# Kernel tuning notes

Measured on AMD Instinct MI355X. Metric: run time of the kernel, lower is better.

## Reference

```python
import jax, jax.numpy as jnp
import numpy as np

DIM, HEADS, DIM_HEAD = 1024, 16, 64
INNER = HEADS * DIM_HEAD  # 1024
FF = 4 * DIM
EPS = 1e-5


def layer_norm(x, g, b):
    mu = jnp.mean(x, axis=-1, keepdims=True)
    var = jnp.mean(jnp.square(x - mu), axis=-1, keepdims=True)
    return (x - mu) * jax.lax.rsqrt(var + EPS) * g + b


def setup_inputs() -> dict:
    key = jax.random.key(0)
    ks = jax.random.split(key, 8)
    B, N = 2, 2048
    s = 0.02
    return {
        "x": jax.random.normal(ks[0], (B, N, DIM), dtype=jnp.float32),
        "ln1_g": jnp.ones((DIM,), jnp.float32),
        "ln1_b": jnp.zeros((DIM,), jnp.float32),
        "ln2_g": jnp.ones((DIM,), jnp.float32),
        "ln2_b": jnp.zeros((DIM,), jnp.float32),
        "w_qkv": jax.random.normal(ks[1], (DIM, 3 * INNER), jnp.float32) * s,
        "w_out": jax.random.normal(ks[2], (INNER, DIM), jnp.float32) * s,
        "b_out": jnp.zeros((DIM,), jnp.float32),
        "w_ff1": jax.random.normal(ks[3], (DIM, FF), jnp.float32) * s,
        "b_ff1": jnp.zeros((FF,), jnp.float32),
        "w_ff2": jax.random.normal(ks[4], (FF, DIM), jnp.float32) * s,
        "b_ff2": jnp.zeros((DIM,), jnp.float32),
    }


def reference(x, ln1_g, ln1_b, ln2_g, ln2_b, w_qkv, w_out, b_out,
              w_ff1, b_ff1, w_ff2, b_ff2):
    B, N, _ = x.shape
    scale = DIM_HEAD ** -0.5
    h = layer_norm(x, ln1_g, ln1_b)
    qkv = h @ w_qkv  # [B, N, 3*INNER]
    q, k, v = jnp.split(qkv, 3, axis=-1)
    # b n (h d) -> b h n d
    def to_heads(t):
        return t.reshape(B, N, HEADS, DIM_HEAD).transpose(0, 2, 1, 3)
    q, k, v = to_heads(q), to_heads(k), to_heads(v)
    dots = jnp.einsum('bhnd,bhmd->bhnm', q, k) * scale
    attn = jax.nn.softmax(dots, axis=-1)  # dropout = identity (eval)
    out = jnp.einsum('bhnm,bhmd->bhnd', attn, v)
    out = out.transpose(0, 2, 1, 3).reshape(B, N, INNER)
    out = out @ w_out + b_out
    x = x + out  # residual
    h2 = layer_norm(x, ln2_g, ln2_b)
    ff = jax.nn.gelu(h2 @ w_ff1 + b_ff1, approximate=False) @ w_ff2 + b_ff2
    return x + ff
```

## Files before the change

kernel.cpp:

```cpp
#include <hip/hip_runtime.h>
#include <hip/hip_bf16.h>
#include <math.h>

#define SEQ   2048
#define BATCH 2
#define NROWS 4096
#define DIMM  1024
#define QKV3  3072
#define FFD   4096
#define NHEAD 16
#define DHEAD 64

typedef __bf16 bf16;
typedef __bf16 bf16x4 __attribute__((ext_vector_type(4)));
typedef __bf16 bf16x8 __attribute__((ext_vector_type(8)));
typedef float  f32x4  __attribute__((ext_vector_type(4)));

static __device__ __forceinline__ f32x4 mfma16(bf16x8 a, bf16x8 b, f32x4 c) {
    return __builtin_amdgcn_mfma_f32_16x16x32_bf16(a, b, c, 0, 0, 0);
}

#define GLDS16(gp, lp) __builtin_amdgcn_global_load_lds( \
    (__attribute__((address_space(1))) void*)(gp),       \
    (__attribute__((address_space(3))) void*)(lp), 16, 0, 0)

#define MEMFENCE asm volatile("" ::: "memory")

__global__ __launch_bounds__(256) void wcast_kernel(
    const float* __restrict__ wqkv, bf16* __restrict__ wqkvT,
    const float* __restrict__ wout, bf16* __restrict__ woutT,
    const float* __restrict__ wff1, bf16* __restrict__ wff1T,
    const float* __restrict__ wff2, bf16* __restrict__ wff2T)
{
    int t = blockIdx.x;
    const float* src; bf16* dst; int K, N, nx;
    if (t < 3072)      { src = wqkv; dst = wqkvT; K = DIMM; N = QKV3; nx = 96;  }
    else if (t < 4096) { src = wout; dst = woutT; K = DIMM; N = DIMM; nx = 32; t -= 3072; }
    else if (t < 8192) { src = wff1; dst = wff1T; K = DIMM; N = FFD;  nx = 128; t -= 4096; }
    else               { src = wff2; dst = wff2T; K = FFD;  N = DIMM; nx = 32; t -= 8192; }
    const int k0 = (t / nx) * 32;
    const int n0 = (t - (t / nx) * nx) * 32;

    __shared__ float tile[32][33];
    const int r = threadIdx.x >> 5;
    const int c = threadIdx.x & 31;
    #pragma unroll
    for (int i = 0; i < 4; ++i)
        tile[r + 8 * i][c] = src[(size_t)(k0 + r + 8 * i) * N + n0 + c];
    __syncthreads();
    #pragma unroll
    for (int i = 0; i < 4; ++i)
        dst[(size_t)(n0 + r + 8 * i) * K + k0 + c] = (bf16)tile[c][r + 8 * i];
}

__global__ __launch_bounds__(256) void ln_cast_kernel(
    const float* __restrict__ x, const float* __restrict__ g,
    const float* __restrict__ b, bf16* __restrict__ out)
{
    const int row = blockIdx.x;
    const int t = threadIdx.x;
    const float4 v = ((const float4*)(x + (size_t)row * DIMM))[t];
    float s  = v.x + v.y + v.z + v.w;
    float sq = v.x * v.x + v.y * v.y + v.z * v.z + v.w * v.w;
    #pragma unroll
    for (int m = 1; m < 64; m <<= 1) {
        s  += __shfl_xor(s, m, 64);
        sq += __shfl_xor(sq, m, 64);
    }
    __shared__ float ss[4], ssq[4];
    const int wave = t >> 6;
    if ((t & 63) == 0) { ss[wave] = s; ssq[wave] = sq; }
    __syncthreads();
    s  = ss[0] + ss[1] + ss[2] + ss[3];
    sq = ssq[0] + ssq[1] + ssq[2] + ssq[3];
    const float mean = s * (1.0f / DIMM);
    const float var  = sq * (1.0f / DIMM) - mean * mean;
    const float rs   = rsqrtf(var + 1e-5f);
    const float4 gv = ((const float4*)g)[t];
    const float4 bv = ((const float4*)b)[t];
    bf16* o = out + (size_t)row * DIMM + t * 4;
    o[0] = (bf16)((v.x - mean) * rs * gv.x + bv.x);
    o[1] = (bf16)((v.y - mean) * rs * gv.y + bv.y);
    o[2] = (bf16)((v.z - mean) * rs * gv.z + bv.z);
    o[3] = (bf16)((v.w - mean) * rs * gv.w + bv.w);
}

template<int EPI>
__global__ __launch_bounds__(512, 2)
void gemm256_kernel(const bf16* __restrict__ A, const bf16* __restrict__ BT,
                    const float* __restrict__ bias, bf16* __restrict__ C,
                    int M, int N, int K, int ld)
{
    __shared__ bf16 As_[2][2][8192];
    __shared__ bf16 Bs_[2][2][8192];
    const int nb = N >> 8;
    const int chunk = (int)gridDim.x >> 3;
    const int idx = ((int)blockIdx.x & 7) * chunk + ((int)blockIdx.x >> 3);
    const int bm = idx / nb, bn = idx - bm * nb;
    const int tm = bm << 8, tn = bn << 8;
    const int tid = threadIdx.x;
    const int lane = tid & 63, w = tid >> 6;
    const int wr = w >> 2, wc = w & 3;
    const int lq = lane & 15, hk = lane >> 4;

    const int sr  = lane >> 3;
    const int sgo = (((lane & 7) ^ sr) << 3);
    const bf16* gA0 = A  + (size_t)(tm +       w * 8 + sr) * ld + sgo;
    const bf16* gA1 = A  + (size_t)(tm + 128 + w * 8 + sr) * ld + sgo;
    const bf16* gB0 = BT + (size_t)(tn +       w * 8 + sr) * ld + sgo;
    const bf16* gB1 = BT + (size_t)(tn + 128 + w * 8 + sr) * ld + sgo;
    const size_t l64 = (size_t)64 * ld;

#define STG_A0(D, T) do { const size_t ko_ = (size_t)(T) * 64;              \
        GLDS16(gA0 + ko_,       &As_[D][0][w * 512]);                       \
        GLDS16(gA0 + ko_ + l64, &As_[D][0][4096 + w * 512]); } while (0)
#define STG_A1(D, T) do { const size_t ko_ = (size_t)(T) * 64;              \
        GLDS16(gA1 + ko_,       &As_[D][1][w * 512]);                       \
        GLDS16(gA1 + ko_ + l64, &As_[D][1][4096 + w * 512]); } while (0)
#define STG_B0(D, T) do { const size_t ko_ = (size_t)(T) * 64;              \
        GLDS16(gB0 + ko_,       &Bs_[D][0][w * 512]);                       \
        GLDS16(gB0 + ko_ + l64, &Bs_[D][0][4096 + w * 512]); } while (0)
#define STG_B1(D, T) do { const size_t ko_ = (size_t)(T) * 64;              \
        GLDS16(gB1 + ko_,       &Bs_[D][1][w * 512]);                       \
        GLDS16(gB1 + ko_ + l64, &Bs_[D][1][4096 + w * 512]); } while (0)

    f32x4 acc[8][4] = {};
    const int NT = K >> 6;

    STG_A0(0, 0); STG_B1(0, 0); STG_B0(0, 0); STG_A1(0, 0);
    STG_B0(1, 1); STG_A1(1, 1);

    for (int t = 0; t < NT; ++t) {
        const int d = t & 1, e = d ^ 1;
        if (t == NT - 1) asm volatile("s_waitcnt vmcnt(0)" ::: "memory");
        else             asm volatile("s_waitcnt vmcnt(4)" ::: "memory");
        __builtin_amdgcn_s_barrier();
        MEMFENCE;

        const char* Ah0 = (const char*)&As_[d][0][0];
        const char* Ah1 = (const char*)&As_[d][1][0];
        const char* Bh0 = (const char*)&Bs_[d][0][0];
        const char* Bh1 = (const char*)&Bs_[d][1][0];
        bf16x8 af[4][2], bfv[2][2];

#define DO_MFMA(MH, NH) do {                                                 \
        __builtin_amdgcn_s_setprio(1);                                       \
        _Pragma("unroll")                                                    \
        for (int mi = 0; mi < 4; ++mi)                                       \
            _Pragma("unroll")                                                \
            for (int nj = 0; nj < 2; ++nj)                                   \
                _Pragma("unroll")                                            \
                for (int kk = 0; kk < 2; ++kk)                               \
                    acc[(MH)*4+mi][(NH)*2+nj] =                              \
                        mfma16(bfv[nj][kk], af[mi][kk], acc[(MH)*4+mi][(NH)*2+nj]); \
        __builtin_amdgcn_s_setprio(0); } while (0)

        {
            #pragma unroll
            for (int mi = 0; mi < 4; ++mi) {
                const int lr = wr * 64 + mi * 16 + lq;
                af[mi][0] = *(const bf16x8*)(Ah0 + lr * 128 + ((hk ^ (lr & 7)) << 4));
                af[mi][1] = *(const bf16x8*)(Ah0 + lr * 128 + (((4 + hk) ^ (lr & 7)) << 4));
            }
            #pragma unroll
            for (int nj = 0; nj < 2; ++nj) {
                const int lc = wc * 32 + nj * 16 + lq;
                bfv[nj][0] = *(const bf16x8*)(Bh0 + lc * 128 + ((hk ^ (lc & 7)) << 4));
                bfv[nj][1] = *(const bf16x8*)(Bh0 + lc * 128 + (((4 + hk) ^ (lc & 7)) << 4));
            }
            if (t + 1 < NT) STG_A0(e, t + 1);
            DO_MFMA(0, 0);
        }
        MEMFENCE; __builtin_amdgcn_s_barrier(); MEMFENCE;
        {
            #pragma unroll
            for (int mi = 0; mi < 4; ++mi) {
                const int lr = wr * 64 + mi * 16 + lq;
                af[mi][0] = *(const bf16x8*)(Ah1 + lr * 128 + ((hk ^ (lr & 7)) << 4));
                af[mi][1] = *(const bf16x8*)(Ah1 + lr * 128 + (((4 + hk) ^ (lr & 7)) << 4));
            }
            if (t + 1 < NT) STG_B1(e, t + 1);
            DO_MFMA(1, 0);
        }
        MEMFENCE; __builtin_amdgcn_s_barrier(); MEMFENCE;
        {
            #pragma unroll
            for (int nj = 0; nj < 2; ++nj) {
                const int lc = wc * 32 + nj * 16 + lq;
                bfv[nj][0] = *(const bf16x8*)(Bh1 + lc * 128 + ((hk ^ (lc & 7)) << 4));
                bfv[nj][1] = *(const bf16x8*)(Bh1 + lc * 128 + (((4 + hk) ^ (lc & 7)) << 4));
            }
            if (t + 2 < NT) STG_B0(d, t + 2);
            DO_MFMA(1, 1);
        }
        MEMFENCE; __builtin_amdgcn_s_barrier(); MEMFENCE;
        {
            #pragma unroll
            for (int mi = 0; mi < 4; ++mi) {
                const int lr = wr * 64 + mi * 16 + lq;
                af[mi][0] = *(const bf16x8*)(Ah0 + lr * 128 + ((hk ^ (lr & 7)) << 4));
                af[mi][1] = *(const bf16x8*)(Ah0 + lr * 128 + (((4 + hk) ^ (lr & 7)) << 4));
            }
            if (t + 2 < NT) STG_A1(d, t + 2);
            DO_MFMA(0, 1);
        }
        MEMFENCE; __builtin_amdgcn_s_barrier(); MEMFENCE;
#undef DO_MFMA
    }
#undef STG_A0
#undef STG_A1
#undef STG_B0
#undef STG_B1

    #pragma unroll
    for (int i = 0; i < 8; ++i) {
        const int mh = i >> 2, mi = i & 3;
        const int row = tm + mh * 128 + wr * 64 + mi * 16 + lq;
        #pragma unroll
        for (int j = 0; j < 4; ++j) {
            const int nh = j >> 1, nj = j & 1;
            const int col = tn + nh * 128 + wc * 32 + nj * 16 + (hk << 2);
            if (EPI == 0) {
                bf16x4 pk = { (bf16)acc[i][j][0], (bf16)acc[i][j][1],
                              (bf16)acc[i][j][2], (bf16)acc[i][j][3] };
                *(bf16x4*)(C + (size_t)row * N + col) = pk;
            } else {
                const float4 bv4 = *(const float4*)(bias + col);
                float v0 = acc[i][j][0] + bv4.x, v1 = acc[i][j][1] + bv4.y;
                float v2 = acc[i][j][2] + bv4.z, v3 = acc[i][j][3] + bv4.w;
                bf16x4 pk = {
                    (bf16)(0.5f * v0 * (1.0f + erff(v0 * 0.70710678118654752f))),
                    (bf16)(0.5f * v1 * (1.0f + erff(v1 * 0.70710678118654752f))),
                    (bf16)(0.5f * v2 * (1.0f + erff(v2 * 0.70710678118654752f))),
                    (bf16)(0.5f * v3 * (1.0f + erff(v3 * 0.70710678118654752f))) };
                *(bf16x4*)(C + (size_t)row * N + col) = pk;
            }
        }
    }
}

template<int EPI>
__global__ __launch_bounds__(256, 3)
void gemm_bt_kernel(const bf16* __restrict__ A, const bf16* __restrict__ BT,
                    const float* __restrict__ bias, const float* __restrict__ res,
                    void* __restrict__ Cout, int M, int N, int K, int ld)
{
    __shared__ bf16 As[3][4096];
    __shared__ bf16 Bs[3][4096];
    const int nb = N >> 7;
    const int chunk = (int)gridDim.x >> 3;
    int idx = (blockIdx.x & 7) * chunk + (blockIdx.x >> 3);
    int ks = 0;
    if (EPI == 3) {
        const int tiles = (M >> 7) * nb;
        ks = idx / tiles;
        idx -= ks * tiles;
    }
    const int bm = idx / nb, bn = idx - bm * nb;
    const int tm = bm << 7, tn = bn << 7;
    const int tid = threadIdx.x;
    const int lane = tid & 63, wave = tid >> 6;
    const int wm = (wave >> 1) << 6, wn = (wave & 1) << 6;
    const int kofs = ks * K;

    const bf16* ga = A  + (size_t)(tm + wave * 32 + (lane >> 2)) * ld + kofs + ((lane & 3) << 3);
    const bf16* gb = BT + (size_t)(tn + wave * 32 + (lane >> 2)) * ld + kofs + ((lane & 3) << 3);
    const size_t k16 = (size_t)16 * ld;

    f32x4 acc[4][4] = {};
    const int ro = (lane & 15) * 32 + ((lane >> 4) << 3);

#define GSTAGE(BUF, KO) do {                          \
        bf16* la_ = &As[BUF][wave * 1024];            \
        bf16* lb_ = &Bs[BUF][wave * 1024];            \
        GLDS16(ga + (KO),       la_);                 \
        GLDS16(ga + (KO) + k16, la_ + 512);           \
        GLDS16(gb + (KO),       lb_);                 \
        GLDS16(gb + (KO) + k16, lb_ + 512);           \
    } while (0)

    GSTAGE(0, 0);
    GSTAGE(1, 32);
    GSTAGE(2, 64);
    int cur = 0;
    for (int k0 = 0; k0 < K; k0 += 32) {
        if (k0 + 96 <= K)      asm volatile("s_waitcnt vmcnt(8)" ::: "memory");
        else if (k0 + 64 <= K) asm volatile("s_waitcnt vmcnt(4)" ::: "memory");
        else                   asm volatile("s_waitcnt vmcnt(0)" ::: "memory");
        __builtin_amdgcn_s_barrier();

        bf16x8 af[4], bfr[4];
        #pragma unroll
        for (int i = 0; i < 4; ++i) {
            af[i]  = *(const bf16x8*)(&As[cur][0] + (wm + i * 16) * 32 + ro);
            bfr[i] = *(const bf16x8*)(&Bs[cur][0] + (wn + i * 16) * 32 + ro);
        }
        #pragma unroll
        for (int i = 0; i < 4; ++i)
            #pragma unroll
            for (int j = 0; j < 4; ++j)
                acc[i][j] = mfma16(bfr[j], af[i], acc[i][j]);

        MEMFENCE;
        __builtin_amdgcn_s_barrier();
        MEMFENCE;
        if (k0 + 96 < K) GSTAGE(cur, k0 + 96);
        cur = (cur == 2) ? 0 : cur + 1;
    }
#undef GSTAGE

    const int lq = lane & 15, hk = lane >> 4;
    const int r0 = tm + wm + lq;
    const int c0 = tn + wn + (hk << 2);
    if (EPI == 0) {
        bf16* C = (bf16*)Cout;
        #pragma unroll
        for (int j = 0; j < 4; ++j)
            #pragma unroll
            for (int i = 0; i < 4; ++i) {
                bf16x4 pk = { (bf16)acc[i][j][0], (bf16)acc[i][j][1],
                              (bf16)acc[i][j][2], (bf16)acc[i][j][3] };
                *(bf16x4*)(C + (size_t)(r0 + i * 16) * N + c0 + j * 16) = pk;
            }
    } else if (EPI == 1) {
        float* C = (float*)Cout;
        #pragma unroll
        for (int j = 0; j < 4; ++j) {
            const float4 bv4 = *(const float4*)(bias + c0 + j * 16);
            #pragma unroll
            for (int i = 0; i < 4; ++i) {
                const size_t off = (size_t)(r0 + i * 16) * N + c0 + j * 16;
                const float4 rv = *(const float4*)(res + off);
                float4 o;
                o.x = acc[i][j][0] + bv4.x + rv.x;
                o.y = acc[i][j][1] + bv4.y + rv.y;
                o.z = acc[i][j][2] + bv4.z + rv.z;
                o.w = acc[i][j][3] + bv4.w + rv.w;
                *(float4*)(C + off) = o;
            }
        }
    } else {
        float* C = (float*)(ks == 0 ? Cout : (void*)res);
        #pragma unroll
        for (int j = 0; j < 4; ++j)
            #pragma unroll
            for (int i = 0; i < 4; ++i) {
                float4 o = { acc[i][j][0], acc[i][j][1], acc[i][j][2], acc[i][j][3] };
                *(float4*)(C + (size_t)(r0 + i * 16) * N + c0 + j * 16) = o;
            }
    }
}

__global__ __launch_bounds__(256) void ff2_reduce_kernel(
    const float* __restrict__ p0, const float* __restrict__ p1,
    const float* __restrict__ bias, const float* __restrict__ res,
    float* __restrict__ out)
{
    const int i = blockIdx.x * 256 + threadIdx.x;
    const float4 a = ((const float4*)p0)[i];
    const float4 b = ((const float4*)p1)[i];
    const float4 r = ((const float4*)res)[i];
    const float4 g = ((const float4*)bias)[i & 255];
    float4 o;
    o.x = a.x + b.x + r.x + g.x;
    o.y = a.y + b.y + r.y + g.y;
    o.z = a.z + b.z + r.z + g.z;
    o.w = a.w + b.w + r.w + g.w;
    ((float4*)out)[i] = o;
}

__global__ __launch_bounds__(256) void vtrans_kernel(
    const bf16* __restrict__ qkv, bf16* __restrict__ vT)
{
    __shared__ bf16 t[64 * 64];
    const int n0 = blockIdx.x * 64;
    const int bh = blockIdx.y;
    const int b = bh >> 4, h = bh & 15;
    const bf16* src = qkv + (size_t)(b * SEQ + n0) * QKV3 + 2 * DIMM + h * DHEAD;

    #pragma unroll
    for (int it = 0; it < 2; ++it) {
        const int c = it * 256 + threadIdx.x;
        const int n = c >> 3, d8 = (c & 7) * 8;
        const bf16x8 v8 = *(const bf16x8*)(src + (size_t)n * QKV3 + d8);
        const int byte = (n * 128 + d8 * 2) ^ (((n >> 3) & 7) << 4);
        *(bf16x8*)((char*)t + byte) = v8;
    }
    __syncthreads();
    #pragma unroll
    for (int it = 0; it < 2; ++it) {
        const int c = it * 256 + threadIdx.x;
        const int d = c >> 3, nc = c & 7;
        bf16x8 o8;
        #pragma unroll
        for (int i = 0; i < 8; ++i) {
            const int n = nc * 8 + i;
            const int byte = (n * 128 + d * 2) ^ ((nc & 7) << 4);
            o8[i] = *(const bf16*)((const char*)t + byte);
        }
        bf16* dstrow = vT + (size_t)bh * DHEAD * SEQ + (size_t)d * SEQ;
        #pragma unroll
        for (int half = 0; half < 2; ++half) {
            const int nb2 = nc * 8 + half * 4;
            const int nabs = n0 + nb2;
            const int off = nb2 & 31;
            const int offp = (((off >> 4) & 1) << 2) | (((off >> 2) & 3) << 3);
            bf16x4 q4 = { o8[half * 4 + 0], o8[half * 4 + 1],
                          o8[half * 4 + 2], o8[half * 4 + 3] };
            *(bf16x4*)(dstrow + (nabs & ~31) + offp) = q4;
        }
    }
}

struct AttnState { float m, l; f32x4 o[4]; };

static __device__ __forceinline__ void attn_body(
    const bf16* __restrict__ Kbuf, const bf16* __restrict__ Vbuf,
    const bf16x8* __restrict__ qf, int q, int hi, AttnState& st)
{
    f32x4 sv[4];
    __builtin_amdgcn_s_setprio(1);
    #pragma unroll
    for (int kf = 0; kf < 4; ++kf) {
        f32x4 z = {0.f, 0.f, 0.f, 0.f};
        sv[kf] = z;
        #pragma unroll
        for (int ks = 0; ks < 2; ++ks) {
            const int row = kf * 16 + q;
            const int bo = (row * 128 + ks * 64 + (hi << 4)) ^ ((row & 7) << 4);
            const bf16x8 kfrag = *(const bf16x8*)((const char*)Kbuf + bo);
            sv[kf] = mfma16(kfrag, qf[ks], sv[kf]);
        }
    }
    __builtin_amdgcn_s_setprio(0);

    float pmax;
    {
        float a = fmaxf(fmaxf(sv[0][0], sv[0][1]), fmaxf(sv[0][2], sv[0][3]));
        float b2 = fmaxf(fmaxf(sv[1][0], sv[1][1]), fmaxf(sv[1][2], sv[1][3]));
        float c = fmaxf(fmaxf(sv[2][0], sv[2][1]), fmaxf(sv[2][2], sv[2][3]));
        float d = fmaxf(fmaxf(sv[3][0], sv[3][1]), fmaxf(sv[3][2], sv[3][3]));
        pmax = fmaxf(fmaxf(a, b2), fmaxf(c, d));
    }
    pmax = fmaxf(pmax, __shfl_xor(pmax, 16, 64));
    pmax = fmaxf(pmax, __shfl_xor(pmax, 32, 64));

    if (__any(pmax - st.m > 8.0f)) {
        const float nm = fmaxf(st.m, pmax);
        const float fr = __expf(st.m - nm);
        st.l *= fr;
        #pragma unroll
        for (int df = 0; df < 4; ++df) {
            st.o[df][0] *= fr; st.o[df][1] *= fr;
            st.o[df][2] *= fr; st.o[df][3] *= fr;
        }
        st.m = nm;
    }

    float pv[4][4];
    float rsum = 0.0f;
    #pragma unroll
    for (int kf = 0; kf < 4; ++kf)
        #pragma unroll
        for (int r = 0; r < 4; ++r) {
            pv[kf][r] = __expf(sv[kf][r] - st.m);
            rsum += pv[kf][r];
        }
    st.l += rsum;

    bf16x8 pb[2];
    #pragma unroll
    for (int ks = 0; ks < 2; ++ks)
        #pragma unroll
        for (int r = 0; r < 4; ++r) {
            pb[ks][r]     = (bf16)pv[2 * ks][r];
            pb[ks][r + 4] = (bf16)pv[2 * ks + 1][r];
        }

    __builtin_amdgcn_s_setprio(1);
    #pragma unroll
    for (int df = 0; df < 4; ++df) {
        const int rowv = df * 16 + q;
        #pragma unroll
        for (int ks = 0; ks < 2; ++ks) {
            const int bo = (rowv * 128 + ks * 64 + (hi << 4)) ^ ((rowv & 7) << 4);
            const bf16x8 vfrag = *(const bf16x8*)((const char*)Vbuf + bo);
            st.o[df] = mfma16(vfrag, pb[ks], st.o[df]);
        }
    }
    __builtin_amdgcn_s_setprio(0);
}

__global__ __launch_bounds__(256, 4)
void attn_kernel(const bf16* __restrict__ qkv, const bf16* __restrict__ vT,
                 bf16* __restrict__ out)
{
    __shared__ bf16 Ks[2][64 * 64];
    __shared__ bf16 Vs[2][64 * 64];
    const int bid = blockIdx.x;
    const int idx = (bid & 7) * 128 + (bid >> 3);
    const int qt = idx & 31;
    const int bh = idx >> 5;
    const int b = bh >> 4, h = bh & 15;
    const int tid = threadIdx.x;
    const int lane = tid & 63, wave = tid >> 6;
    const int q = lane & 15, hi = lane >> 4;

    const bf16* qbase = qkv + (size_t)(b * SEQ) * QKV3 + h * DHEAD;
    const bf16* kbase = qbase + DIMM;
    const bf16* vbase = vT + (size_t)bh * DHEAD * SEQ;

    const int q0 = qt * 64 + wave * 16;
    bf16x8 qf[2];
    {
        const bf16* qp = qbase + (size_t)(q0 + q) * QKV3 + (hi << 3);
        qf[0] = *(const bf16x8*)qp;
        qf[1] = *(const bf16x8*)(qp + 32);
        #pragma unroll
        for (int j = 0; j < 8; ++j) {
            qf[0][j] = (bf16)((float)qf[0][j] * 0.125f);
            qf[1][j] = (bf16)((float)qf[1][j] * 0.125f);
        }
    }

    const int srow = lane >> 3;
    const int scol = ((lane & 7) ^ srow) << 3;
    const bf16* gk = kbase + (size_t)(wave * 16 + srow) * QKV3 + scol;
    const bf16* gv = vbase + (size_t)(wave * 16 + srow) * SEQ + scol;

#define STAGE(BUF, KT) do {                                        \
        bf16* lk_ = &Ks[BUF][wave * 1024];                         \
        bf16* lv_ = &Vs[BUF][wave * 1024];                         \
        GLDS16(gk + (size_t)(KT) * QKV3,       lk_);               \
        GLDS16(gk + (size_t)((KT) + 8) * QKV3, lk_ + 512);         \
        GLDS16(gv + (KT),                      lv_);               \
        GLDS16(gv + (KT) + 8 * SEQ,            lv_ + 512);         \
    } while (0)

    AttnState st;
    st.m = -1e30f; st.l = 0.0f;
    #pragma unroll
    for (int df = 0; df < 4; ++df) {
        f32x4 z = {0.f, 0.f, 0.f, 0.f};
        st.o[df] = z;
    }

    STAGE(0, 0);
    for (int kt = 0; kt < SEQ; kt += 128) {
        __syncthreads();
        STAGE(1, kt + 64);
        attn_body(&Ks[0][0], &Vs[0][0], qf, q, hi, st);
        __syncthreads();
        if (kt + 128 < SEQ) STAGE(0, kt + 128);
        attn_body(&Ks[1][0], &Vs[1][0], qf, q, hi, st);
    }
#undef STAGE

    {
        float lt = st.l;
        lt += __shfl_xor(lt, 16, 64);
        lt += __shfl_xor(lt, 32, 64);
        const float inv = 1.0f / lt;
        const int grow = b * SEQ + q0 + q;
        #pragma unroll
        for (int df = 0; df < 4; ++df) {
            bf16x4 pk = { (bf16)(st.o[df][0] * inv), (bf16)(st.o[df][1] * inv),
                          (bf16)(st.o[df][2] * inv), (bf16)(st.o[df][3] * inv) };
            *(bf16x4*)(out + (size_t)grow * DIMM + h * DHEAD + df * 16 + hi * 4) = pk;
        }
    }
}

extern "C" void kernel_launch(void* const* d_in, const int* in_sizes, int n_in,
                              void* d_out, int out_size, void* d_ws, size_t ws_size,
                              hipStream_t stream)
{
    (void)in_sizes; (void)n_in; (void)out_size;
    const float* x    = (const float*)d_in[0];
    const float* ln1g = (const float*)d_in[1];
    const float* ln1b = (const float*)d_in[2];
    const float* ln2g = (const float*)d_in[3];
    const float* ln2b = (const float*)d_in[4];
    const float* wqkv = (const float*)d_in[5];
    const float* wout = (const float*)d_in[6];
    const float* bout = (const float*)d_in[7];
    const float* wff1 = (const float*)d_in[8];
    const float* bff1 = (const float*)d_in[9];
    const float* wff2 = (const float*)d_in[10];
    const float* bff2 = (const float*)d_in[11];

    char* ws = (char*)d_ws;
    const dim3 blk(256);
    const dim3 blk512(512);
    const bool splitk = ws_size >= 92274688ULL;

    if (splitk) {
        bf16*  wff2T = (bf16*)(ws);
        bf16*  woutT = (bf16*)(ws + 8388608);
        bf16*  wff1T = (bf16*)(ws + 10485760);
        bf16*  wqkvT = (bf16*)(ws + 18874368);
        bf16*  hbuf  = (bf16*)(ws + 25165824);
        bf16*  qkvb  = (bf16*)(ws + 33554432);
        bf16*  vT    = (bf16*)(ws + 58720256);
        bf16*  attnb = (bf16*)(ws + 67108864);
        float* x2    = (float*)(ws + 75497472);
        bf16*  fbuf  = (bf16*)(ws + 41943040);
        float* p0    = (float*)(ws + 8388608);
        float* p1    = (float*)(ws + 25165824);

        wcast_kernel<<<dim3(12288), blk, 0, stream>>>(
            wqkv, wqkvT, wout, woutT, wff1, wff1T, wff2, wff2T);

        ln_cast_kernel<<<NROWS, blk, 0, stream>>>(x, ln1g, ln1b, hbuf);
        gemm_bt_kernel<0><<<(NROWS / 128) * (QKV3 / 128), blk, 0, stream>>>(
            hbuf, wqkvT, nullptr, nullptr, qkvb, NROWS, QKV3, DIMM, DIMM);
        vtrans_kernel<<<dim3(SEQ / 64, BATCH * NHEAD), blk, 0, stream>>>(qkvb, vT);
        attn_kernel<<<dim3(1024), blk, 0, stream>>>(qkvb, vT, attnb);
        gemm_bt_kernel<1><<<(NROWS / 128) * (DIMM / 128), blk, 0, stream>>>(
            attnb, woutT, bout, x, x2, NROWS, DIMM, DIMM, DIMM);
        ln_cast_kernel<<<NROWS, blk, 0, stream>>>(x2, ln2g, ln2b, hbuf);
        gemm256_kernel<2><<<(NROWS / 256) * (FFD / 256), blk512, 0, stream>>>(
            hbuf, wff1T, bff1, fbuf, NROWS, FFD, DIMM, DIMM);
        gemm_bt_kernel<3><<<2 * (NROWS / 128) * (DIMM / 128), blk, 0, stream>>>(
            fbuf, wff2T, nullptr, (const float*)p1, p0, NROWS, DIMM, FFD / 2, FFD);
        ff2_reduce_kernel<<<(NROWS * DIMM) / 1024, blk, 0, stream>>>(
            p0, p1, bff2, x2, (float*)d_out);
    } else {
        bf16*  wqkvT = (bf16*)(ws);
        bf16*  woutT = (bf16*)(ws + 6291456);
        bf16*  wff1T = (bf16*)(ws + 8388608);
        bf16*  wff2T = (bf16*)(ws + 16777216);
        float* x2    = (float*)(ws + 25165824);
        bf16*  vT    = (bf16*)(ws + 25165824);
        bf16*  hbuf  = (bf16*)(ws + 41943040);
        bf16*  qkvb  = (bf16*)(ws + 50331648);
        bf16*  attnb = (bf16*)(ws + 75497472);
        bf16*  fbuf  = (bf16*)(ws + 50331648);

        wcast_kernel<<<dim3(12288), blk, 0, stream>>>(
            wqkv, wqkvT, wout, woutT, wff1, wff1T, wff2, wff2T);

        ln_cast_kernel<<<NROWS, blk, 0, stream>>>(x, ln1g, ln1b, hbuf);
        gemm_bt_kernel<0><<<(NROWS / 128) * (QKV3 / 128), blk, 0, stream>>>(
            hbuf, wqkvT, nullptr, nullptr, qkvb, NROWS, QKV3, DIMM, DIMM);
        vtrans_kernel<<<dim3(SEQ / 64, BATCH * NHEAD), blk, 0, stream>>>(qkvb, vT);
        attn_kernel<<<dim3(1024), blk, 0, stream>>>(qkvb, vT, attnb);
        gemm_bt_kernel<1><<<(NROWS / 128) * (DIMM / 128), blk, 0, stream>>>(
            attnb, woutT, bout, x, x2, NROWS, DIMM, DIMM, DIMM);
        ln_cast_kernel<<<NROWS, blk, 0, stream>>>(x2, ln2g, ln2b, hbuf);
        gemm256_kernel<2><<<(NROWS / 256) * (FFD / 256), blk512, 0, stream>>>(
            hbuf, wff1T, bff1, fbuf, NROWS, FFD, DIMM, DIMM);
        gemm_bt_kernel<1><<<(NROWS / 128) * (DIMM / 128), blk, 0, stream>>>(
            fbuf, wff2T, bff2, x2, (float*)d_out, NROWS, DIMM, FFD, FFD);
    }
}
```

Measured before the change: 255.0 us.

## Process two 16-row query fragments per wave in attention to reuse K/V fragments

Each attention wave now handles 32 query rows, as two 16-row MFMA fragments, instead of 16. Every K and V fragment read from LDS then feeds two MFMAs, which halves LDS traffic and K/V staging per query row. Each block covers 128 query rows, so the grid drops from 1024 to 512 blocks and launch bounds go from 4 to 2 blocks per CU. The trade-off is higher register pressure and fewer resident waves to hide latency, on a grid that is now only 512 blocks.

```diff
diff --git a/kernel.cpp b/kernel.cpp
--- a/kernel.cpp
+++ b/kernel.cpp
@@ -412,70 +412,74 @@
     }
 }
 
-struct AttnState { float m, l; f32x4 o[4]; };
-
-static __device__ __forceinline__ void attn_body(
+struct AttnState2 { float m[2], l[2]; f32x4 o[2][4]; };
+
+static __device__ __forceinline__ void attn_body2(
     const bf16* __restrict__ Kbuf, const bf16* __restrict__ Vbuf,
-    const bf16x8* __restrict__ qf, int q, int hi, AttnState& st)
-{
-    f32x4 sv[4];
+    const bf16x8 qf[2][2], int q, int hi, AttnState2& st)
+{
+    f32x4 sv[2][4];
     __builtin_amdgcn_s_setprio(1);
     #pragma unroll
     for (int kf = 0; kf < 4; ++kf) {
         f32x4 z = {0.f, 0.f, 0.f, 0.f};
-        sv[kf] = z;
+        sv[0][kf] = z; sv[1][kf] = z;
         #pragma unroll
         for (int ks = 0; ks < 2; ++ks) {
             const int row = kf * 16 + q;
             const int bo = (row * 128 + ks * 64 + (hi << 4)) ^ ((row & 7) << 4);
             const bf16x8 kfrag = *(const bf16x8*)((const char*)Kbuf + bo);
-            sv[kf] = mfma16(kfrag, qf[ks], sv[kf]);
+            sv[0][kf] = mfma16(kfrag, qf[0][ks], sv[0][kf]);
+            sv[1][kf] = mfma16(kfrag, qf[1][ks], sv[1][kf]);
         }
     }
     __builtin_amdgcn_s_setprio(0);
 
-    float pmax;
-    {
-        float a = fmaxf(fmaxf(sv[0][0], sv[0][1]), fmaxf(sv[0][2], sv[0][3]));
-        float b2 = fmaxf(fmaxf(sv[1][0], sv[1][1]), fmaxf(sv[1][2], sv[1][3]));
-        float c = fmaxf(fmaxf(sv[2][0], sv[2][1]), fmaxf(sv[2][2], sv[2][3]));
-        float d = fmaxf(fmaxf(sv[3][0], sv[3][1]), fmaxf(sv[3][2], sv[3][3]));
-        pmax = fmaxf(fmaxf(a, b2), fmaxf(c, d));
-    }
-    pmax = fmaxf(pmax, __shfl_xor(pmax, 16, 64));
-    pmax = fmaxf(pmax, __shfl_xor(pmax, 32, 64));
-
-    if (__any(pmax - st.m > 8.0f)) {
-        const float nm = fmaxf(st.m, pmax);
-        const float fr = __expf(st.m - nm);
-        st.l *= fr;
-        #pragma unroll
-        for (int df = 0; df < 4; ++df) {
-            st.o[df][0] *= fr; st.o[df][1] *= fr;
-            st.o[df][2] *= fr; st.o[df][3] *= fr;
-        }
-        st.m = nm;
-    }
-
-    float pv[4][4];
-    float rsum = 0.0f;
-    #pragma unroll
-    for (int kf = 0; kf < 4; ++kf)
-        #pragma unroll
-        for (int r = 0; r < 4; ++r) {
-            pv[kf][r] = __expf(sv[kf][r] - st.m);
-            rsum += pv[kf][r];
-        }
-    st.l += rsum;
-
-    bf16x8 pb[2];
-    #pragma unroll
-    for (int ks = 0; ks < 2; ++ks)
-        #pragma unroll
-        for (int r = 0; r < 4; ++r) {
-            pb[ks][r]     = (bf16)pv[2 * ks][r];
-            pb[ks][r + 4] = (bf16)pv[2 * ks + 1][r];
-        }
+    bf16x8 pb[2][2];
+    #pragma unroll
+    for (int mf = 0; mf < 2; ++mf) {
+        float pmax;
+        {
+            float a = fmaxf(fmaxf(sv[mf][0][0], sv[mf][0][1]), fmaxf(sv[mf][0][2], sv[mf][0][3]));
+            float b2 = fmaxf(fmaxf(sv[mf][1][0], sv[mf][1][1]), fmaxf(sv[mf][1][2], sv[mf][1][3]));
+            float c = fmaxf(fmaxf(sv[mf][2][0], sv[mf][2][1]), fmaxf(sv[mf][2][2], sv[mf][2][3]));
+            float d = fmaxf(fmaxf(sv[mf][3][0], sv[mf][3][1]), fmaxf(sv[mf][3][2], sv[mf][3][3]));
+            pmax = fmaxf(fmaxf(a, b2), fmaxf(c, d));
+        }
+        pmax = fmaxf(pmax, __shfl_xor(pmax, 16, 64));
+        pmax = fmaxf(pmax, __shfl_xor(pmax, 32, 64));
+
+        if (__any(pmax - st.m[mf] > 8.0f)) {
+            const float nm = fmaxf(st.m[mf], pmax);
+            const float fr = __expf(st.m[mf] - nm);
+            st.l[mf] *= fr;
+            #pragma unroll
+            for (int df = 0; df < 4; ++df) {
+                st.o[mf][df][0] *= fr; st.o[mf][df][1] *= fr;
+                st.o[mf][df][2] *= fr; st.o[mf][df][3] *= fr;
+            }
+            st.m[mf] = nm;
+        }
+
+        float pv[4][4];
+        float rsum = 0.0f;
+        #pragma unroll
+        for (int kf = 0; kf < 4; ++kf)
+            #pragma unroll
+            for (int r = 0; r < 4; ++r) {
+                pv[kf][r] = __expf(sv[mf][kf][r] - st.m[mf]);
+                rsum += pv[kf][r];
+            }
+        st.l[mf] += rsum;
+
+        #pragma unroll
+        for (int ks = 0; ks < 2; ++ks)
+            #pragma unroll
+            for (int r = 0; r < 4; ++r) {
+                pb[mf][ks][r]     = (bf16)pv[2 * ks][r];
+                pb[mf][ks][r + 4] = (bf16)pv[2 * ks + 1][r];
+            }
+    }
 
     __builtin_amdgcn_s_setprio(1);
     #pragma unroll
@@ -485,22 +489,23 @@
         for (int ks = 0; ks < 2; ++ks) {
             const int bo = (rowv * 128 + ks * 64 + (hi << 4)) ^ ((rowv & 7) << 4);
             const bf16x8 vfrag = *(const bf16x8*)((const char*)Vbuf + bo);
-            st.o[df] = mfma16(vfrag, pb[ks], st.o[df]);
+            st.o[0][df] = mfma16(vfrag, pb[0][ks], st.o[0][df]);
+            st.o[1][df] = mfma16(vfrag, pb[1][ks], st.o[1][df]);
         }
     }
     __builtin_amdgcn_s_setprio(0);
 }
 
-__global__ __launch_bounds__(256, 4)
+__global__ __launch_bounds__(256, 2)
 void attn_kernel(const bf16* __restrict__ qkv, const bf16* __restrict__ vT,
                  bf16* __restrict__ out)
 {
     __shared__ bf16 Ks[2][64 * 64];
     __shared__ bf16 Vs[2][64 * 64];
     const int bid = blockIdx.x;
-    const int idx = (bid & 7) * 128 + (bid >> 3);
-    const int qt = idx & 31;
-    const int bh = idx >> 5;
+    const int idx = (bid & 7) * 64 + (bid >> 3);
+    const int qt = idx & 15;
+    const int bh = idx >> 4;
     const int b = bh >> 4, h = bh & 15;
     const int tid = threadIdx.x;
     const int lane = tid & 63, wave = tid >> 6;
@@ -510,16 +515,17 @@
     const bf16* kbase = qbase + DIMM;
     const bf16* vbase = vT + (size_t)bh * DHEAD * SEQ;
 
-    const int q0 = qt * 64 + wave * 16;
-    bf16x8 qf[2];
-    {
-        const bf16* qp = qbase + (size_t)(q0 + q) * QKV3 + (hi << 3);
-        qf[0] = *(const bf16x8*)qp;
-        qf[1] = *(const bf16x8*)(qp + 32);
+    const int q0 = qt * 128 + wave * 32;
+    bf16x8 qf[2][2];
+    #pragma unroll
+    for (int mf = 0; mf < 2; ++mf) {
+        const bf16* qp = qbase + (size_t)(q0 + mf * 16 + q) * QKV3 + (hi << 3);
+        qf[mf][0] = *(const bf16x8*)qp;
+        qf[mf][1] = *(const bf16x8*)(qp + 32);
         #pragma unroll
         for (int j = 0; j < 8; ++j) {
-            qf[0][j] = (bf16)((float)qf[0][j] * 0.125f);
-            qf[1][j] = (bf16)((float)qf[1][j] * 0.125f);
+            qf[mf][0][j] = (bf16)((float)qf[mf][0][j] * 0.125f);
+            qf[mf][1][j] = (bf16)((float)qf[mf][1][j] * 0.125f);
         }
     }
 
@@ -537,35 +543,39 @@
         GLDS16(gv + (KT) + 8 * SEQ,            lv_ + 512);         \
     } while (0)
 
-    AttnState st;
-    st.m = -1e30f; st.l = 0.0f;
-    #pragma unroll
-    for (int df = 0; df < 4; ++df) {
-        f32x4 z = {0.f, 0.f, 0.f, 0.f};
-        st.o[df] = z;
+    AttnState2 st;
+    #pragma unroll
+    for (int mf = 0; mf < 2; ++mf) {
+        st.m[mf] = -1e30f; st.l[mf] = 0.0f;
+        #pragma unroll
+        for (int df = 0; df < 4; ++df) {
+            f32x4 z = {0.f, 0.f, 0.f, 0.f};
+            st.o[mf][df] = z;
+        }
     }
 
     STAGE(0, 0);
     for (int kt = 0; kt < SEQ; kt += 128) {
         __syncthreads();
         STAGE(1, kt + 64);
-        attn_body(&Ks[0][0], &Vs[0][0], qf, q, hi, st);
+        attn_body2(&Ks[0][0], &Vs[0][0], qf, q, hi, st);
         __syncthreads();
         if (kt + 128 < SEQ) STAGE(0, kt + 128);
-        attn_body(&Ks[1][0], &Vs[1][0], qf, q, hi, st);
+        attn_body2(&Ks[1][0], &Vs[1][0], qf, q, hi, st);
     }
 #undef STAGE
 
-    {
-        float lt = st.l;
+    #pragma unroll
+    for (int mf = 0; mf < 2; ++mf) {
+        float lt = st.l[mf];
         lt += __shfl_xor(lt, 16, 64);
         lt += __shfl_xor(lt, 32, 64);
         const float inv = 1.0f / lt;
-        const int grow = b * SEQ + q0 + q;
+        const int grow = b * SEQ + q0 + mf * 16 + q;
         #pragma unroll
         for (int df = 0; df < 4; ++df) {
-            bf16x4 pk = { (bf16)(st.o[df][0] * inv), (bf16)(st.o[df][1] * inv),
-                          (bf16)(st.o[df][2] * inv), (bf16)(st.o[df][3] * inv) };
+            bf16x4 pk = { (bf16)(st.o[mf][df][0] * inv), (bf16)(st.o[mf][df][1] * inv),
+                          (bf16)(st.o[mf][df][2] * inv), (bf16)(st.o[mf][df][3] * inv) };
             *(bf16x4*)(out + (size_t)grow * DIMM + h * DHEAD + df * 16 + hi * 4) = pk;
         }
     }
@@ -615,7 +625,7 @@
         gemm_bt_kernel<0><<<(NROWS / 128) * (QKV3 / 128), blk, 0, stream>>>(
             hbuf, wqkvT, nullptr, nullptr, qkvb, NROWS, QKV3, DIMM, DIMM);
         vtrans_kernel<<<dim3(SEQ / 64, BATCH * NHEAD), blk, 0, stream>>>(qkvb, vT);
-        attn_kernel<<<dim3(1024), blk, 0, stream>>>(qkvb, vT, attnb);
+        attn_kernel<<<dim3(512), blk, 0, stream>>>(qkvb, vT, attnb);
         gemm_bt_kernel<1><<<(NROWS / 128) * (DIMM / 128), blk, 0, stream>>>(
             attnb, woutT, bout, x, x2, NROWS, DIMM, DIMM, DIMM);
         ln_cast_kernel<<<NROWS, blk, 0, stream>>>(x2, ln2g, ln2b, hbuf);
@@ -644,7 +654,7 @@
         gemm_bt_kernel<0><<<(NROWS / 128) * (QKV3 / 128), blk, 0, stream>>>(
             hbuf, wqkvT, nullptr, nullptr, qkvb, NROWS, QKV3, DIMM, DIMM);
         vtrans_kernel<<<dim3(SEQ / 64, BATCH * NHEAD), blk, 0, stream>>>(qkvb, vT);
-        attn_kernel<<<dim3(1024), blk, 0, stream>>>(qkvb, vT, attnb);
+        attn_kernel<<<dim3(512), blk, 0, stream>>>(qkvb, vT, attnb);
         gemm_bt_kernel<1><<<(NROWS / 128) * (DIMM / 128), blk, 0, stream>>>(
             attnb, woutT, bout, x, x2, NROWS, DIMM, DIMM, DIMM);
         ln_cast_kernel<<<NROWS, blk, 0, stream>>>(x2, ln2g, ln2b, hbuf);
```

New measurement: 255.8 us. Within noise of the previous version (+0.3%).
